# Optimization experiments

Hardware: AMD Instinct MI355X
Metric: run time of the kernel (lower is better)

Reference implementation:

```python
import jax, jax.numpy as jnp
import numpy as np

D_MODEL = 768
NUM_HEADS = 12
D_K = D_MODEL // NUM_HEADS


def setup_inputs() -> dict:
    key = jax.random.key(0)
    ks = jax.random.split(key, 11)
    B, S, D = 2, 4096, D_MODEL
    scale = 1.0 / np.sqrt(D)
    return {
        "Q": jax.random.normal(ks[0], (B, S, D), jnp.float32),
        "K": jax.random.normal(ks[1], (B, S, D), jnp.float32),
        "V": jax.random.normal(ks[2], (B, S, D), jnp.float32),
        "Wq": jax.random.normal(ks[3], (D, D), jnp.float32) * scale,
        "bq": jnp.zeros((D,), jnp.float32),
        "Wk": jax.random.normal(ks[4], (D, D), jnp.float32) * scale,
        "bk": jnp.zeros((D,), jnp.float32),
        "Wv": jax.random.normal(ks[5], (D, D), jnp.float32) * scale,
        "bv": jnp.zeros((D,), jnp.float32),
        "Wo": jax.random.normal(ks[6], (D, D), jnp.float32) * scale,
        "bo": jnp.zeros((D,), jnp.float32),
    }


def _split_heads(x):
    # (B, S, D) -> (B, H, S, d_k)
    B, S, _ = x.shape
    return x.reshape(B, S, NUM_HEADS, D_K).transpose(0, 2, 1, 3)


def reference(Q, K, V, Wq, bq, Wk, bk, Wv, bv, Wo, bo):
    # Linear projections (torch Linear: x @ W.T + b)
    q = _split_heads(Q @ Wq.T + bq)  # (B,H,S,dk)
    k = _split_heads(K @ Wk.T + bk)
    v = _split_heads(V @ Wv.T + bv)
    # Naive unfused attention: materialize full (B,H,S,S) scores
    scores = jnp.einsum("bhqd,bhkd->bhqk", q, k) / jnp.sqrt(jnp.float32(D_K))
    probs = jax.nn.softmax(scores, axis=-1)
    attn = jnp.einsum("bhqk,bhkd->bhqd", probs, v)  # (B,H,S,dk)
    B, H, S, dk = attn.shape
    combined = attn.transpose(0, 2, 1, 3).reshape(B, S, H * dk)
    return combined @ Wo.T + bo
```

## Files before the change

kernel.cpp:

```cpp
#include <hip/hip_runtime.h>
#include <hip/hip_bf16.h>
#include <stdint.h>

#define D_MODEL 768
#define NHEAD 12
#define DK 64
#define SQ 4096
#define BATCH 2
#define MROWS (BATCH*SQ)
#define WELEMS (D_MODEL*D_MODEL)
#define XELEMS ((size_t)MROWS*D_MODEL)
#define TENS_ELEMS ((size_t)BATCH*NHEAD*SQ*DK)

#define QSCALE 0.1803368801111244f

typedef __attribute__((ext_vector_type(8))) unsigned short u16x8;
typedef __attribute__((ext_vector_type(4))) unsigned short u16x4;
typedef __attribute__((ext_vector_type(4))) unsigned int   u32x4;
typedef __attribute__((ext_vector_type(8))) __bf16 bf16x8;
typedef __attribute__((ext_vector_type(4))) float f32x4;
typedef __attribute__((ext_vector_type(16))) float f32x16;

__device__ __forceinline__ unsigned short f2bfu(float f){
    uint32_t u = __float_as_uint(f);
    return (unsigned short)((u + 0x7fffu + ((u >> 16) & 1u)) >> 16);
}

__device__ __forceinline__ bf16x8 load_bf8(const unsigned short* p){
    u16x8 t = *reinterpret_cast<const u16x8*>(p);
    return __builtin_bit_cast(bf16x8, t);
}

__device__ __forceinline__ unsigned cvtpk(float lo, float hi){
    unsigned r;
    asm("v_cvt_pk_bf16_f32 %0, %1, %2" : "=v"(r) : "v"(lo), "v"(hi));
    return r;
}

__device__ __forceinline__ float exp2_hw(float x){
    float r;
    asm("v_exp_f32 %0, %1" : "=v"(r) : "v"(x));
    return r;
}

__device__ __forceinline__ f32x16 zero16(){
    f32x16 z;
    #pragma unroll
    for (int i = 0; i < 16; ++i) z[i] = 0.f;
    return z;
}

__global__ __launch_bounds__(256) void wconv_kernel(const float* w0, const float* w1,
                                                    const float* w2, const float* w3,
                                                    unsigned short* dst){
    const float* src = (blockIdx.y == 0) ? w0 : (blockIdx.y == 1) ? w1 :
                       (blockIdx.y == 2) ? w2 : w3;
    unsigned short* d = dst + (size_t)blockIdx.y * WELEMS;
    int i = (blockIdx.x * blockDim.x + threadIdx.x) * 4;
    if (i < WELEMS){
        float4 v = *reinterpret_cast<const float4*>(src + i);
        u16x4 o;
        o[0]=f2bfu(v.x); o[1]=f2bfu(v.y); o[2]=f2bfu(v.z); o[3]=f2bfu(v.w);
        *reinterpret_cast<u16x4*>(d + i) = o;
    }
}

__global__ __launch_bounds__(256) void xconv_kernel(const float* src, unsigned short* dst){
    size_t i = ((size_t)blockIdx.x * blockDim.x + threadIdx.x) * 4;
    float4 v = *reinterpret_cast<const float4*>(src + i);
    u16x4 o;
    o[0]=f2bfu(v.x); o[1]=f2bfu(v.y); o[2]=f2bfu(v.z); o[3]=f2bfu(v.w);
    *reinterpret_cast<u16x4*>(dst + i) = o;
}

template<int MODE>
__global__ __launch_bounds__(256) void gemm_kernel(const unsigned short* A, const unsigned short* Wb,
                                                   const float* bias, float oscale, void* out_){
    const int wave = threadIdx.x >> 6, lane = threadIdx.x & 63;
    const int g = lane >> 4, c16 = lane & 15;
    const int m0 = blockIdx.x * 64 + wave * 16;
    const int n0 = blockIdx.y * 64;
    f32x4 acc[4];
    #pragma unroll
    for (int c = 0; c < 4; ++c) acc[c] = f32x4{0.f,0.f,0.f,0.f};
    const unsigned short* ap = A  + (size_t)(m0 + c16) * D_MODEL + g * 8;
    const unsigned short* bp = Wb + (size_t)(n0 + c16) * D_MODEL + g * 8;
    #pragma unroll 4
    for (int kc = 0; kc < D_MODEL; kc += 32){
        bf16x8 af = load_bf8(ap + kc);
        #pragma unroll
        for (int c = 0; c < 4; ++c){
            bf16x8 bfr = load_bf8(bp + (size_t)(c*16) * D_MODEL + kc);
            acc[c] = __builtin_amdgcn_mfma_f32_16x16x32_bf16(af, bfr, acc[c], 0, 0, 0);
        }
    }
    #pragma unroll
    for (int c = 0; c < 4; ++c){
        const int n = n0 + c*16 + c16;
        const float bv = bias[n];
        #pragma unroll
        for (int r = 0; r < 4; ++r){
            const int mrow = m0 + g*4 + r;
            const float v = (acc[c][r] + bv) * oscale;
            if constexpr (MODE == 3){
                ((float*)out_)[(size_t)mrow * D_MODEL + n] = v;
            } else {
                const int b = mrow >> 12, s = mrow & 4095;
                const int h = n >> 6, d = n & 63;
                unsigned short* o = (unsigned short*)out_;
                if constexpr (MODE == 2){
                    o[((size_t)(b*NHEAD + h)*DK + d)*SQ + s] = f2bfu(v);
                } else {
                    o[((size_t)(b*NHEAD + h)*SQ + s)*DK + d] = f2bfu(v);
                }
            }
        }
    }
}

__global__ __launch_bounds__(256) void attn_kernel(const unsigned short* q, const unsigned short* k,
                                                   const unsigned short* vt, unsigned short* att){
    const int lane = threadIdx.x & 63;
    const int wave = threadIdx.x >> 6;
    const int c32 = lane & 31, hi = lane >> 5;
    const int bh = blockIdx.y;
    const int b = bh / NHEAD, h = bh % NHEAD;
    const int q0 = blockIdx.x * 128 + wave * 32;
    const unsigned short* qb = q + ((size_t)bh * SQ + q0) * DK;

    const unsigned short* kp = k  + (size_t)bh * SQ * DK + (size_t)c32 * DK + hi * 8;
    const unsigned short* vp = vt + (size_t)bh * DK * SQ + (size_t)c32 * SQ + hi * 8;

    bf16x8 qf[4];
    #pragma unroll
    for (int ks = 0; ks < 4; ++ks)
        qf[ks] = load_bf8(qb + (size_t)c32 * DK + ks*16 + hi*8);

    f32x16 o[2];
    o[0] = zero16(); o[1] = zero16();
    float lrow = 0.f;

    for (int it = 0; it < SQ/64; ++it, kp += 64*DK, vp += 64){
        bf16x8 kf[2][4], vf[2][4];
        #pragma unroll
        for (int t = 0; t < 2; ++t)
            #pragma unroll
            for (int ks = 0; ks < 4; ++ks)
                kf[t][ks] = load_bf8(kp + t*32*DK + ks*16);
        #pragma unroll
        for (int f = 0; f < 4; ++f)
            vf[0][f] = load_bf8(vp + f*16);

        f32x16 sc[2];
        sc[0] = zero16(); sc[1] = zero16();
        __builtin_amdgcn_s_setprio(1);
        #pragma unroll
        for (int ks = 0; ks < 4; ++ks){
            sc[0] = __builtin_amdgcn_mfma_f32_32x32x16_bf16(kf[0][ks], qf[ks], sc[0], 0, 0, 0);
            sc[1] = __builtin_amdgcn_mfma_f32_32x32x16_bf16(kf[1][ks], qf[ks], sc[1], 0, 0, 0);
        }
        __builtin_amdgcn_s_setprio(0);

        #pragma unroll
        for (int f = 0; f < 4; ++f)
            vf[1][f] = load_bf8(vp + (size_t)32*SQ + f*16);

        float ps[16];
        #pragma unroll
        for (int r = 0; r < 16; ++r){
            float p0 = exp2_hw(sc[0][r]);
            float p1 = exp2_hw(sc[1][r]);
            sc[0][r] = p0; sc[1][r] = p1;
            ps[r] = p0 + p1;
        }
        #pragma unroll
        for (int s = 8; s > 0; s >>= 1)
            #pragma unroll
            for (int r = 0; r < 8; ++r)
                if (r < s) ps[r] += ps[r + s];
        lrow += ps[0];

        unsigned Wd[2][4][2];
        #pragma unroll
        for (int t = 0; t < 2; ++t)
            #pragma unroll
            for (int gq = 0; gq < 4; ++gq){
                Wd[t][gq][0] = cvtpk(sc[t][gq*4+0], sc[t][gq*4+1]);
                Wd[t][gq][1] = cvtpk(sc[t][gq*4+2], sc[t][gq*4+3]);
            }
        unsigned Rv[2][2][2];
        #pragma unroll
        for (int t = 0; t < 2; ++t)
            #pragma unroll
            for (int gp = 0; gp < 2; ++gp)
                #pragma unroll
                for (int w = 0; w < 2; ++w){
                    unsigned snd = hi ? Wd[t][2*gp][w] : Wd[t][2*gp+1][w];
                    Rv[t][gp][w] = (unsigned)__shfl_xor((int)snd, 32, 64);
                }
        bf16x8 paf[4];
        #pragma unroll
        for (int t = 0; t < 2; ++t)
            #pragma unroll
            for (int gp = 0; gp < 2; ++gp){
                const int f = t*2 + gp;
                u32x4 wd;
                wd[0] = hi ? Rv[t][gp][0]     : Wd[t][2*gp][0];
                wd[1] = hi ? Rv[t][gp][1]     : Wd[t][2*gp][1];
                wd[2] = hi ? Wd[t][2*gp+1][0] : Rv[t][gp][0];
                wd[3] = hi ? Wd[t][2*gp+1][1] : Rv[t][gp][1];
                paf[f] = __builtin_bit_cast(bf16x8, wd);
            }

        __builtin_amdgcn_s_setprio(1);
        #pragma unroll
        for (int f = 0; f < 4; ++f){
            o[0] = __builtin_amdgcn_mfma_f32_32x32x16_bf16(paf[f], vf[0][f], o[0], 0, 0, 0);
            o[1] = __builtin_amdgcn_mfma_f32_32x32x16_bf16(paf[f], vf[1][f], o[1], 0, 0, 0);
        }
        __builtin_amdgcn_s_setprio(0);
    }

    float ltot = lrow + __shfl_xor(lrow, 32, 64);
    float linv = 1.0f / ltot;
    float li[16];
    #pragma unroll
    for (int r = 0; r < 16; ++r)
        li[r] = __shfl(linv, (r&3) + 8*(r>>2) + 4*hi, 64);
    #pragma unroll
    for (int td = 0; td < 2; ++td)
        #pragma unroll
        for (int r = 0; r < 16; ++r){
            const int qrow = (r&3) + 8*(r>>2) + 4*hi;
            att[((size_t)(b*SQ + q0 + qrow)) * D_MODEL + h*DK + td*32 + c32] =
                f2bfu(o[td][r] * li[r]);
        }
}

extern "C" void kernel_launch(void* const* d_in, const int* in_sizes, int n_in,
                              void* d_out, int out_size, void* d_ws, size_t ws_size,
                              hipStream_t stream){
    const float* Q  = (const float*)d_in[0];
    const float* K  = (const float*)d_in[1];
    const float* V  = (const float*)d_in[2];
    const float* Wq = (const float*)d_in[3];
    const float* bq = (const float*)d_in[4];
    const float* Wk = (const float*)d_in[5];
    const float* bk = (const float*)d_in[6];
    const float* Wv = (const float*)d_in[7];
    const float* bv = (const float*)d_in[8];
    const float* Wo = (const float*)d_in[9];
    const float* bo = (const float*)d_in[10];
    float* out = (float*)d_out;

    unsigned short* q_ws   = (unsigned short*)d_ws;
    unsigned short* k_ws   = q_ws  + TENS_ELEMS;
    unsigned short* vt_ws  = k_ws  + TENS_ELEMS;
    unsigned short* att_ws = vt_ws + TENS_ELEMS;
    unsigned short* wbf    = att_ws + TENS_ELEMS;
    unsigned short* xbf    = wbf + 4*WELEMS;

    wconv_kernel<<<dim3(576, 4), 256, 0, stream>>>(Wq, Wk, Wv, Wo, wbf);

    xconv_kernel<<<6144, 256, 0, stream>>>(Q, xbf);
    gemm_kernel<0><<<dim3(128, 12), 256, 0, stream>>>(xbf, wbf,            bq, QSCALE, q_ws);
    xconv_kernel<<<6144, 256, 0, stream>>>(K, xbf);
    gemm_kernel<1><<<dim3(128, 12), 256, 0, stream>>>(xbf, wbf + WELEMS,   bk, 1.0f,   k_ws);
    xconv_kernel<<<6144, 256, 0, stream>>>(V, xbf);
    gemm_kernel<2><<<dim3(128, 12), 256, 0, stream>>>(xbf, wbf + 2*WELEMS, bv, 1.0f,   vt_ws);

    attn_kernel<<<dim3(32, 24), 256, 0, stream>>>(q_ws, k_ws, vt_ws, att_ws);

    gemm_kernel<3><<<dim3(128, 12), 256, 0, stream>>>(att_ws, wbf + 3*WELEMS, bo, 1.0f, out);
}
```

Measured before the change: 807.1 us.

## Double GEMM row tile per wave and remap attention blocks by XCD

Each GEMM wave now computes two 16-row tiles, so every B-fragment load feeds two MFMAs. This halves the GEMM grid and cuts weight reloads from global memory. The attention launch becomes a flat 1D grid whose block index is decoded so that blocks on the same XCD (L & 7) share the same batch-head. That keeps the K and V streams local to one L2. The cost is more registers in the GEMM and fewer GEMM blocks to fill the GPU.

```diff
diff --git a/kernel.cpp b/kernel.cpp
--- a/kernel.cpp
+++ b/kernel.cpp
@@ -78,40 +78,45 @@
                                                    const float* bias, float oscale, void* out_){
     const int wave = threadIdx.x >> 6, lane = threadIdx.x & 63;
     const int g = lane >> 4, c16 = lane & 15;
-    const int m0 = blockIdx.x * 64 + wave * 16;
+    const int m0 = blockIdx.x * 128 + wave * 32;
     const int n0 = blockIdx.y * 64;
-    f32x4 acc[4];
-    #pragma unroll
-    for (int c = 0; c < 4; ++c) acc[c] = f32x4{0.f,0.f,0.f,0.f};
-    const unsigned short* ap = A  + (size_t)(m0 + c16) * D_MODEL + g * 8;
-    const unsigned short* bp = Wb + (size_t)(n0 + c16) * D_MODEL + g * 8;
-    #pragma unroll 4
+    f32x4 acc[2][4];
+    #pragma unroll
+    for (int rt = 0; rt < 2; ++rt)
+        #pragma unroll
+        for (int c = 0; c < 4; ++c) acc[rt][c] = f32x4{0.f,0.f,0.f,0.f};
     for (int kc = 0; kc < D_MODEL; kc += 32){
-        bf16x8 af = load_bf8(ap + kc);
+        const int kk = kc + g * 8;
+        bf16x8 a0 = load_bf8(A + (size_t)(m0 + c16) * D_MODEL + kk);
+        bf16x8 a1 = load_bf8(A + (size_t)(m0 + 16 + c16) * D_MODEL + kk);
         #pragma unroll
         for (int c = 0; c < 4; ++c){
-            bf16x8 bfr = load_bf8(bp + (size_t)(c*16) * D_MODEL + kc);
-            acc[c] = __builtin_amdgcn_mfma_f32_16x16x32_bf16(af, bfr, acc[c], 0, 0, 0);
-        }
-    }
-    #pragma unroll
-    for (int c = 0; c < 4; ++c){
-        const int n = n0 + c*16 + c16;
-        const float bv = bias[n];
-        #pragma unroll
-        for (int r = 0; r < 4; ++r){
-            const int mrow = m0 + g*4 + r;
-            const float v = (acc[c][r] + bv) * oscale;
-            if constexpr (MODE == 3){
-                ((float*)out_)[(size_t)mrow * D_MODEL + n] = v;
-            } else {
-                const int b = mrow >> 12, s = mrow & 4095;
-                const int h = n >> 6, d = n & 63;
-                unsigned short* o = (unsigned short*)out_;
-                if constexpr (MODE == 2){
-                    o[((size_t)(b*NHEAD + h)*DK + d)*SQ + s] = f2bfu(v);
+            bf16x8 bfr = load_bf8(Wb + (size_t)(n0 + c*16 + c16) * D_MODEL + kk);
+            acc[0][c] = __builtin_amdgcn_mfma_f32_16x16x32_bf16(a0, bfr, acc[0][c], 0, 0, 0);
+            acc[1][c] = __builtin_amdgcn_mfma_f32_16x16x32_bf16(a1, bfr, acc[1][c], 0, 0, 0);
+        }
+    }
+    #pragma unroll
+    for (int rt = 0; rt < 2; ++rt){
+        #pragma unroll
+        for (int c = 0; c < 4; ++c){
+            const int n = n0 + c*16 + c16;
+            const float bv = bias[n];
+            #pragma unroll
+            for (int r = 0; r < 4; ++r){
+                const int mrow = m0 + rt*16 + g*4 + r;
+                const float v = (acc[rt][c][r] + bv) * oscale;
+                if constexpr (MODE == 3){
+                    ((float*)out_)[(size_t)mrow * D_MODEL + n] = v;
                 } else {
-                    o[((size_t)(b*NHEAD + h)*SQ + s)*DK + d] = f2bfu(v);
+                    const int b = mrow >> 12, s = mrow & 4095;
+                    const int h = n >> 6, d = n & 63;
+                    unsigned short* o = (unsigned short*)out_;
+                    if constexpr (MODE == 2){
+                        o[((size_t)(b*NHEAD + h)*DK + d)*SQ + s] = f2bfu(v);
+                    } else {
+                        o[((size_t)(b*NHEAD + h)*SQ + s)*DK + d] = f2bfu(v);
+                    }
                 }
             }
         }
@@ -123,9 +128,12 @@
     const int lane = threadIdx.x & 63;
     const int wave = threadIdx.x >> 6;
     const int c32 = lane & 31, hi = lane >> 5;
-    const int bh = blockIdx.y;
-    const int b = bh / NHEAD, h = bh % NHEAD;
-    const int q0 = blockIdx.x * 128 + wave * 32;
+    const int L = blockIdx.x;
+    const int xcd = L & 7, within = L >> 3;
+    const int bh = xcd * 3 + (within >> 5);
+    const int bq = within & 31;
+    const int b = bh / NHEAD, h = bh - b * NHEAD;
+    const int q0 = bq * 128 + wave * 32;
     const unsigned short* qb = q + ((size_t)bh * SQ + q0) * DK;
 
     const unsigned short* kp = k  + (size_t)bh * SQ * DK + (size_t)c32 * DK + hi * 8;
@@ -263,13 +271,13 @@
     wconv_kernel<<<dim3(576, 4), 256, 0, stream>>>(Wq, Wk, Wv, Wo, wbf);
 
     xconv_kernel<<<6144, 256, 0, stream>>>(Q, xbf);
-    gemm_kernel<0><<<dim3(128, 12), 256, 0, stream>>>(xbf, wbf,            bq, QSCALE, q_ws);
+    gemm_kernel<0><<<dim3(64, 12), 256, 0, stream>>>(xbf, wbf,            bq, QSCALE, q_ws);
     xconv_kernel<<<6144, 256, 0, stream>>>(K, xbf);
-    gemm_kernel<1><<<dim3(128, 12), 256, 0, stream>>>(xbf, wbf + WELEMS,   bk, 1.0f,   k_ws);
+    gemm_kernel<1><<<dim3(64, 12), 256, 0, stream>>>(xbf, wbf + WELEMS,   bk, 1.0f,   k_ws);
     xconv_kernel<<<6144, 256, 0, stream>>>(V, xbf);
-    gemm_kernel<2><<<dim3(128, 12), 256, 0, stream>>>(xbf, wbf + 2*WELEMS, bv, 1.0f,   vt_ws);
-
-    attn_kernel<<<dim3(32, 24), 256, 0, stream>>>(q_ws, k_ws, vt_ws, att_ws);
-
-    gemm_kernel<3><<<dim3(128, 12), 256, 0, stream>>>(att_ws, wbf + 3*WELEMS, bo, 1.0f, out);
-}
+    gemm_kernel<2><<<dim3(64, 12), 256, 0, stream>>>(xbf, wbf + 2*WELEMS, bv, 1.0f,   vt_ws);
+
+    attn_kernel<<<768, 256, 0, stream>>>(q_ws, k_ws, vt_ws, att_ws);
+
+    gemm_kernel<3><<<dim3(64, 12), 256, 0, stream>>>(att_ws, wbf + 3*WELEMS, bo, 1.0f, out);
+}
```

New measurement: 689.4 us. 14.6% less time.
